# Kernel optimization log

Measured on AMD Instinct MI355X. Metric: run time of the kernel, lower is better.

Reference implementation:

```python
import jax, jax.numpy as jnp
import numpy as np

B_, C, N, M, DX = 4, 8, 1024, 1024, 1
POINTS_PER_UNIT = 64


def setup_inputs() -> dict:
    key = jax.random.key(0)
    k1, k2, k3 = jax.random.split(key, 3)
    xz = jax.random.uniform(k1, (M, DX), dtype=jnp.float32)          # grid locations
    z = jax.random.normal(k2, (B_, C, M, M), dtype=jnp.float32)      # grid encoding
    x = jax.random.normal(k3, (B_, N, DX), dtype=jnp.float32)        # target locations
    log_scale = jnp.log(jnp.float32(2.0 / POINTS_PER_UNIT))          # learned scalar
    return {"xz": xz, "z": z, "x": x, "log_scale": log_scale}


def reference(xz, z, x, log_scale):
    # pairwise squared distances: (b, n, m)
    dists2 = jnp.sum((x[:, :, None, :] - xz[None, None, :, :]) ** 2, axis=-1)
    # RBF weights
    weights = jnp.exp(-0.5 * dists2 / jnp.exp(2.0 * log_scale))      # (b, n, m)
    # weighted interpolation of grid encoding: (b, c, n, m)
    z1 = jnp.einsum("bnm,bcmk->bcnk", weights, z)
    # outer product z1 @ z1^T: (b, c, n, n)
    z2 = jnp.einsum("bcnk,bcok->bcno", z1, z1)
    return (xz, z2)
```

## Files before the change

kernel.cpp:

```cpp
#include <hip/hip_runtime.h>
#include <hip/hip_bf16.h>


typedef __attribute__((ext_vector_type(8))) unsigned short u16x8;
typedef __attribute__((ext_vector_type(8))) __bf16 bf16x8;
typedef __attribute__((ext_vector_type(4))) float f32x4;

typedef __attribute__((address_space(1))) void gvoid;
typedef __attribute__((address_space(3))) void svoid;
#define GLDS(g, s) __builtin_amdgcn_global_load_lds((gvoid*)(g), (svoid*)(s), 16, 0, 0)
#define BAR() asm volatile("s_barrier" ::: "memory")

__device__ __forceinline__ unsigned short f2bf(float f) {
  unsigned int u = __builtin_bit_cast(unsigned int, f);
  u += 0x7fffu + ((u >> 16) & 1u);
  return (unsigned short)(u >> 16);
}

__device__ __forceinline__ bf16x8 as_bf16x8(u16x8 v) {
  return __builtin_bit_cast(bf16x8, v);
}

__global__ void weights_kernel(const float* __restrict__ xz, const float* __restrict__ x,
                               const float* __restrict__ ls, unsigned short* __restrict__ W) {
  int bn = blockIdx.x;
  float xv = x[bn];
  float coef = -0.5f * __expf(-2.0f * ls[0]);
  unsigned short* Wrow = W + (size_t)bn * 1024;
  #pragma unroll
  for (int i = 0; i < 4; ++i) {
    int m = threadIdx.x + i * 256;
    float d = xv - xz[m];
    Wrow[m] = f2bf(__expf(coef * d * d));
  }
}

__global__ void transpose_kernel(const float* __restrict__ Z, unsigned short* __restrict__ Zt) {
  __shared__ float tile[64][65];
  int bc = blockIdx.z;
  const float* Zp = Z + ((size_t)bc << 20);
  unsigned short* Ztp = Zt + ((size_t)bc << 20);
  int m0 = blockIdx.x * 64, k0 = blockIdx.y * 64;
  int tx = threadIdx.x & 63, tg = threadIdx.x >> 6;
  #pragma unroll
  for (int i = 0; i < 16; ++i) {
    int ml = tg + i * 4;
    tile[ml][tx] = Zp[(size_t)(m0 + ml) * 1024 + k0 + tx];
  }
  __syncthreads();
  int tx2 = (threadIdx.x & 31) * 2, kg = threadIdx.x >> 5;
  #pragma unroll
  for (int i = 0; i < 8; ++i) {
    int kl = kg + i * 8;
    ushort2 v;
    v.x = f2bf(tile[tx2][kl]);
    v.y = f2bf(tile[tx2 + 1][kl]);
    *(ushort2*)&Ztp[(size_t)(k0 + kl) * 1024 + m0 + tx2] = v;
  }
}

template<bool OUT_BF16, bool A_PER_B>
__global__ __launch_bounds__(512, 2)
void gemm_nt8(const unsigned short* __restrict__ A, const unsigned short* __restrict__ B,
              unsigned short* __restrict__ Cbf, float* __restrict__ Cf) {
  extern __shared__ __align__(16) char smem[];

  const int bid = blockIdx.x;
  const int w = ((bid & 7) << 6) + (bid >> 3);
  const int bc = w >> 4;
  const int t  = w & 15;
  const int bi = t & 3, bj = t >> 2;

  const unsigned short* Ap = A + ((size_t)(A_PER_B ? (bc >> 3) : bc) << 20);
  const unsigned short* Bp = B + ((size_t)bc << 20);
  const int tid = threadIdx.x;
  const int wv = tid >> 6, lane = tid & 63;
  const int wr = wv >> 2, wc = wv & 3;
  const int la = lane & 15, ha = lane >> 4;

  f32x4 acc[8][4] = {};

  const unsigned short* gA0 = Ap + (size_t)(bi*256 +       wv*16 + (lane>>2)) * 1024 + (lane&3)*8;
  const unsigned short* gA1 = Ap + (size_t)(bi*256 + 128 + wv*16 + (lane>>2)) * 1024 + (lane&3)*8;
  const unsigned short* gB0 = Bp + (size_t)(bj*256 +       wv*16 + (lane>>2)) * 1024 + (lane&3)*8;
  const unsigned short* gB1 = Bp + (size_t)(bj*256 + 128 + wv*16 + (lane>>2)) * 1024 + (lane&3)*8;
  const int ldsw = wv * 1024;

  auto stageA = [&](int d, int kh, int kt) {
    const int ko = kt * 64 + kh * 32;
    char* dst = smem + d * 32768 + kh * 16384 + ldsw;
    GLDS(gA0 + ko, dst); GLDS(gA1 + ko, dst + 8192);
  };
  auto stageB = [&](int d, int kh, int kt) {
    const int ko = kt * 64 + kh * 32;
    char* dst = smem + 65536 + d * 32768 + kh * 16384 + ldsw;
    GLDS(gB0 + ko, dst); GLDS(gB1 + ko, dst + 8192);
  };

  const int abase = (wr * 128 + la) * 64 + ha * 16;
  const int bbase = 65536 + (wc * 64 + la) * 64 + ha * 16;

  u16x8 af[4], bfr[4];
  auto lda = [&](int d, int kh, int ms) {
    const char* p = smem + d * 32768 + kh * 16384 + ms * 4096 + abase;
    af[0] = *(const u16x8*)(p);
    af[1] = *(const u16x8*)(p + 1024);
    af[2] = *(const u16x8*)(p + 2048);
    af[3] = *(const u16x8*)(p + 3072);
  };
  auto ldb = [&](int d, int kh) {
    const char* p = smem + d * 32768 + kh * 16384 + bbase;
    bfr[0] = *(const u16x8*)(p);
    bfr[1] = *(const u16x8*)(p + 1024);
    bfr[2] = *(const u16x8*)(p + 2048);
    bfr[3] = *(const u16x8*)(p + 3072);
  };
  auto mfma16 = [&](int ms) {
    __builtin_amdgcn_s_setprio(1);
    #pragma unroll
    for (int i = 0; i < 4; ++i)
      #pragma unroll
      for (int n = 0; n < 4; ++n)
        acc[ms * 4 + i][n] = __builtin_amdgcn_mfma_f32_16x16x32_bf16(
            as_bf16x8(af[i]), as_bf16x8(bfr[n]), acc[ms * 4 + i][n], 0, 0, 0);
    __builtin_amdgcn_s_setprio(0);
  };

  stageA(0, 0, 0); stageB(0, 0, 0);
  stageA(0, 1, 0); stageB(0, 1, 0);
  stageA(1, 0, 1); stageB(1, 0, 1);
  asm volatile("s_waitcnt vmcnt(8)" ::: "memory");
  BAR();

  for (int tt = 0; tt < 16; ++tt) {
    const int d = tt & 1;
    if (tt < 15) stageA(d ^ 1, 1, tt + 1);
    ldb(d, 0); lda(d, 0, 0);
    BAR();
    mfma16(0);
    BAR();
    if (tt < 15) stageB(d ^ 1, 1, tt + 1);
    lda(d, 0, 1);
    BAR();
    mfma16(1);
    if (tt < 15) { asm volatile("s_waitcnt vmcnt(8)" ::: "memory"); }
    else         { asm volatile("s_waitcnt vmcnt(0)" ::: "memory"); }
    BAR();
    if (tt < 14) stageA(d, 0, tt + 2);
    ldb(d, 1); lda(d, 1, 0);
    BAR();
    mfma16(0);
    BAR();
    if (tt < 14) stageB(d, 0, tt + 2);
    lda(d, 1, 1);
    BAR();
    mfma16(1);
    if (tt < 14)       { asm volatile("s_waitcnt vmcnt(8)" ::: "memory"); }
    else if (tt == 14) { asm volatile("s_waitcnt vmcnt(4)" ::: "memory"); }
    BAR();
  }

  const size_t cb20 = (size_t)bc << 20;

  if (OUT_BF16) {
    unsigned short* sE = (unsigned short*)(smem) + wv * 1152;
    const int r2 = lane >> 2, ch = lane & 3;
    #pragma unroll
    for (int mb = 0; mb < 8; ++mb) {
      #pragma unroll
      for (int nb = 0; nb < 4; ++nb)
        #pragma unroll
        for (int j = 0; j < 4; ++j)
          sE[(ha * 4 + j) * 72 + nb * 16 + la] = f2bf(acc[mb][nb][j]);
      u16x8 v0 = *(const u16x8*)&sE[r2 * 72 + ch * 16];
      u16x8 v1 = *(const u16x8*)&sE[r2 * 72 + ch * 16 + 8];
      unsigned short* gp = Cbf + cb20 +
          (size_t)(bi * 256 + wr * 128 + mb * 16 + r2) * 1024 + bj * 256 + wc * 64 + ch * 16;
      *(u16x8*)gp = v0;
      *(u16x8*)(gp + 8) = v1;
    }
  } else {
    #pragma unroll
    for (int mb = 0; mb < 8; ++mb) {
      #pragma unroll
      for (int nb = 0; nb < 4; ++nb) {
        const int col = bj * 256 + wc * 64 + nb * 16 + la;
        #pragma unroll
        for (int j = 0; j < 4; ++j) {
          const int row = bi * 256 + wr * 128 + mb * 16 + ha * 4 + j;
          Cf[cb20 + (size_t)row * 1024 + col] = acc[mb][nb][j];
        }
      }
    }
  }
}

extern "C" void kernel_launch(void* const* d_in, const int* in_sizes, int n_in,
                              void* d_out, int out_size, void* d_ws, size_t ws_size,
                              hipStream_t stream) {
  const float* xz = (const float*)d_in[0];
  const float* z  = (const float*)d_in[1];
  const float* x  = (const float*)d_in[2];
  const float* ls = (const float*)d_in[3];
  float* out = (float*)d_out;

  unsigned short* W  = (unsigned short*)d_ws;
  unsigned short* Zt = W + ((size_t)4 << 20);
  unsigned short* z1 = Zt + ((size_t)32 << 20);

  hipFuncSetAttribute((const void*)gemm_nt8<true,  true >,
                      hipFuncAttributeMaxDynamicSharedMemorySize, 131072);
  hipFuncSetAttribute((const void*)gemm_nt8<false, false>,
                      hipFuncAttributeMaxDynamicSharedMemorySize, 131072);

  hipMemcpyAsync(out, xz, 1024 * sizeof(float), hipMemcpyDeviceToDevice, stream);
  weights_kernel<<<4096, 256, 0, stream>>>(xz, x, ls, W);
  transpose_kernel<<<dim3(16, 16, 32), 256, 0, stream>>>(z, Zt);
  gemm_nt8<true,  true ><<<512, 512, 131072, stream>>>(W,  Zt, z1, nullptr);
  gemm_nt8<false, false><<<512, 512, 131072, stream>>>(z1, z1, nullptr, out + 1024);
}
```

Measured before the change: 195.2 us.

## Exploit symmetry of z1·z1ᵀ with a dedicated upper-triangle GEMM and mirrored stores

Replaces the second full GEMM with a kernel that computes only the upper-triangular 256x128 tiles of each symmetric output and writes each off-diagonal tile twice, once transposed through LDS. This cuts the MFMA work of the second GEMM roughly in half. The fp32 epilogue now goes through LDS for vectorized, coalesced stores instead of scattered scalar writes. The cost is a smaller, differently shaped tile (256 threads, 48KB LDS, a full vmcnt(0) wait each k-step) and extra transpose stores for mirrored tiles.

```diff
diff --git a/kernel.cpp b/kernel.cpp
--- a/kernel.cpp
+++ b/kernel.cpp
@@ -59,10 +59,10 @@
   }
 }
 
-template<bool OUT_BF16, bool A_PER_B>
+template<bool A_PER_B>
 __global__ __launch_bounds__(512, 2)
 void gemm_nt8(const unsigned short* __restrict__ A, const unsigned short* __restrict__ B,
-              unsigned short* __restrict__ Cbf, float* __restrict__ Cf) {
+              unsigned short* __restrict__ Cbf) {
   extern __shared__ __align__(16) char smem[];
 
   const int bid = blockIdx.x;
@@ -136,61 +136,152 @@
     const int d = tt & 1;
     if (tt < 15) stageA(d ^ 1, 1, tt + 1);
     ldb(d, 0); lda(d, 0, 0);
-    BAR();
-    mfma16(0);
-    BAR();
+    BAR(); mfma16(0); BAR();
     if (tt < 15) stageB(d ^ 1, 1, tt + 1);
     lda(d, 0, 1);
-    BAR();
-    mfma16(1);
+    BAR(); mfma16(1);
     if (tt < 15) { asm volatile("s_waitcnt vmcnt(8)" ::: "memory"); }
     else         { asm volatile("s_waitcnt vmcnt(0)" ::: "memory"); }
     BAR();
     if (tt < 14) stageA(d, 0, tt + 2);
     ldb(d, 1); lda(d, 1, 0);
-    BAR();
-    mfma16(0);
-    BAR();
+    BAR(); mfma16(0); BAR();
     if (tt < 14) stageB(d, 0, tt + 2);
     lda(d, 1, 1);
-    BAR();
-    mfma16(1);
+    BAR(); mfma16(1);
     if (tt < 14)       { asm volatile("s_waitcnt vmcnt(8)" ::: "memory"); }
     else if (tt == 14) { asm volatile("s_waitcnt vmcnt(4)" ::: "memory"); }
     BAR();
   }
 
   const size_t cb20 = (size_t)bc << 20;
-
-  if (OUT_BF16) {
-    unsigned short* sE = (unsigned short*)(smem) + wv * 1152;
-    const int r2 = lane >> 2, ch = lane & 3;
-    #pragma unroll
-    for (int mb = 0; mb < 8; ++mb) {
+  unsigned short* sE = (unsigned short*)(smem) + wv * 1152;
+  const int r2 = lane >> 2, ch = lane & 3;
+  #pragma unroll
+  for (int mb = 0; mb < 8; ++mb) {
+    #pragma unroll
+    for (int nb = 0; nb < 4; ++nb)
+      #pragma unroll
+      for (int j = 0; j < 4; ++j)
+        sE[(ha * 4 + j) * 72 + nb * 16 + la] = f2bf(acc[mb][nb][j]);
+    u16x8 v0 = *(const u16x8*)&sE[r2 * 72 + ch * 16];
+    u16x8 v1 = *(const u16x8*)&sE[r2 * 72 + ch * 16 + 8];
+    unsigned short* gp = Cbf + cb20 +
+        (size_t)(bi * 256 + wr * 128 + mb * 16 + r2) * 1024 + bj * 256 + wc * 64 + ch * 16;
+    *(u16x8*)gp = v0;
+    *(u16x8*)(gp + 8) = v1;
+  }
+}
+
+__global__ __launch_bounds__(256, 2)
+void gemm2_sym(const unsigned short* __restrict__ Z1, float* __restrict__ Cf) {
+  __shared__ __align__(16) char smem[49152];
+
+  const int chunk = 80;
+  int w = ((int)blockIdx.x & 7) * chunk + ((int)blockIdx.x >> 3);
+  const int bc = w / 20;
+  int t = w % 20;
+  int bi = 0, cnt = 8;
+  while (t >= cnt) { t -= cnt; ++bi; cnt -= 2; }
+  const int bj = t + 2 * bi;
+  const bool pure = (bj >= 2 * bi + 2);
+
+  const unsigned short* Ap = Z1 + ((size_t)bc << 20);
+  const int tid = threadIdx.x;
+  const int wv = tid >> 6, lane = tid & 63;
+  const int wr = wv >> 1, wc = wv & 1;
+  const int la = lane & 15, ha = lane >> 4;
+
+  f32x4 acc[8][4] = {};
+
+  const int srow = wv * 16 + (lane >> 2);
+  const int scol = (lane & 3) * 8;
+  const unsigned short* gA = Ap + (size_t)(bi * 256 + srow) * 1024 + scol;
+  const unsigned short* gB = Ap + (size_t)(bj * 128 + srow) * 1024 + scol;
+  char* dA = smem + wv * 1024;
+  char* dB = smem + 32768 + wv * 1024;
+
+  auto stage = [&](int d, int tt2) {
+    const int ko = tt2 * 32;
+    GLDS(gA + ko,               dA + d * 16384);
+    GLDS(gA + ko +  64 * 1024,  dA + d * 16384 + 4096);
+    GLDS(gA + ko + 128 * 1024,  dA + d * 16384 + 8192);
+    GLDS(gA + ko + 192 * 1024,  dA + d * 16384 + 12288);
+    GLDS(gB + ko,               dB + d * 8192);
+    GLDS(gB + ko +  64 * 1024,  dB + d * 8192 + 4096);
+  };
+
+  const int abase = wr * 8192 + la * 64 + ha * 16;
+  const int bbase = 32768 + (wc * 64 + la) * 64 + ha * 16;
+  u16x8 af[4], bfr[4];
+  auto lda = [&](int d, int ms) {
+    const char* p = smem + d * 16384 + ms * 4096 + abase;
+    af[0] = *(const u16x8*)(p);
+    af[1] = *(const u16x8*)(p + 1024);
+    af[2] = *(const u16x8*)(p + 2048);
+    af[3] = *(const u16x8*)(p + 3072);
+  };
+  auto ldb = [&](int d) {
+    const char* p = smem + d * 8192 + bbase;
+    bfr[0] = *(const u16x8*)(p);
+    bfr[1] = *(const u16x8*)(p + 1024);
+    bfr[2] = *(const u16x8*)(p + 2048);
+    bfr[3] = *(const u16x8*)(p + 3072);
+  };
+  auto mfma16 = [&](int ms) {
+    __builtin_amdgcn_s_setprio(1);
+    #pragma unroll
+    for (int i = 0; i < 4; ++i)
+      #pragma unroll
+      for (int n = 0; n < 4; ++n)
+        acc[ms * 4 + i][n] = __builtin_amdgcn_mfma_f32_16x16x32_bf16(
+            as_bf16x8(af[i]), as_bf16x8(bfr[n]), acc[ms * 4 + i][n], 0, 0, 0);
+    __builtin_amdgcn_s_setprio(0);
+  };
+
+  stage(0, 0);
+  asm volatile("s_waitcnt vmcnt(0)" ::: "memory");
+  BAR();
+  for (int tt2 = 0; tt2 < 32; ++tt2) {
+    const int d = tt2 & 1;
+    if (tt2 < 31) stage(d ^ 1, tt2 + 1);
+    ldb(d); lda(d, 0);
+    BAR(); mfma16(0); BAR();
+    lda(d, 1);
+    BAR(); mfma16(1);
+    if (tt2 < 31) asm volatile("s_waitcnt vmcnt(0)" ::: "memory");
+    BAR();
+  }
+
+  const size_t cb20 = (size_t)bc << 20;
+  float* sF = (float*)(smem + wv * 12288);
+  float* sM = (float*)(smem + wv * 12288 + 6144);
+  const int rr = lane >> 2, cch = (lane & 3) * 16;
+
+  #pragma unroll
+  for (int mb = 0; mb < 8; ++mb) {
+    #pragma unroll
+    for (int nb = 0; nb < 4; ++nb)
+      #pragma unroll
+      for (int j = 0; j < 4; ++j)
+        sF[(ha * 4 + j) * 68 + nb * 16 + la] = acc[mb][nb][j];
+    float* gp = Cf + cb20 +
+        (size_t)(bi * 256 + wr * 128 + mb * 16 + rr) * 1024 + bj * 128 + wc * 64 + cch;
+    #pragma unroll
+    for (int q = 0; q < 4; ++q)
+      *(f32x4*)(gp + q * 4) = *(const f32x4*)&sF[rr * 68 + cch + q * 4];
+
+    if (pure) {
       #pragma unroll
       for (int nb = 0; nb < 4; ++nb)
         #pragma unroll
         for (int j = 0; j < 4; ++j)
-          sE[(ha * 4 + j) * 72 + nb * 16 + la] = f2bf(acc[mb][nb][j]);
-      u16x8 v0 = *(const u16x8*)&sE[r2 * 72 + ch * 16];
-      u16x8 v1 = *(const u16x8*)&sE[r2 * 72 + ch * 16 + 8];
-      unsigned short* gp = Cbf + cb20 +
-          (size_t)(bi * 256 + wr * 128 + mb * 16 + r2) * 1024 + bj * 256 + wc * 64 + ch * 16;
-      *(u16x8*)gp = v0;
-      *(u16x8*)(gp + 8) = v1;
-    }
-  } else {
-    #pragma unroll
-    for (int mb = 0; mb < 8; ++mb) {
-      #pragma unroll
-      for (int nb = 0; nb < 4; ++nb) {
-        const int col = bj * 256 + wc * 64 + nb * 16 + la;
-        #pragma unroll
-        for (int j = 0; j < 4; ++j) {
-          const int row = bi * 256 + wr * 128 + mb * 16 + ha * 4 + j;
-          Cf[cb20 + (size_t)row * 1024 + col] = acc[mb][nb][j];
-        }
-      }
+          sM[(nb * 16 + la) * 20 + ha * 4 + j] = acc[mb][nb][j];
+      float* mp = Cf + cb20 +
+          (size_t)(bj * 128 + wc * 64 + lane) * 1024 + bi * 256 + wr * 128 + mb * 16;
+      #pragma unroll
+      for (int q = 0; q < 4; ++q)
+        *(f32x4*)(mp + q * 4) = *(const f32x4*)&sM[lane * 20 + q * 4];
     }
   }
 }
@@ -208,14 +299,12 @@
   unsigned short* Zt = W + ((size_t)4 << 20);
   unsigned short* z1 = Zt + ((size_t)32 << 20);
 
-  hipFuncSetAttribute((const void*)gemm_nt8<true,  true >,
-                      hipFuncAttributeMaxDynamicSharedMemorySize, 131072);
-  hipFuncSetAttribute((const void*)gemm_nt8<false, false>,
+  hipFuncSetAttribute((const void*)gemm_nt8<true>,
                       hipFuncAttributeMaxDynamicSharedMemorySize, 131072);
 
   hipMemcpyAsync(out, xz, 1024 * sizeof(float), hipMemcpyDeviceToDevice, stream);
   weights_kernel<<<4096, 256, 0, stream>>>(xz, x, ls, W);
   transpose_kernel<<<dim3(16, 16, 32), 256, 0, stream>>>(z, Zt);
-  gemm_nt8<true,  true ><<<512, 512, 131072, stream>>>(W,  Zt, z1, nullptr);
-  gemm_nt8<false, false><<<512, 512, 131072, stream>>>(z1, z1, nullptr, out + 1024);
-}
+  gemm_nt8<true><<<512, 512, 131072, stream>>>(W, Zt, z1);
+  gemm2_sym<<<640, 256, 0, stream>>>(z1, out + 1024);
+}
```

Result: slower. 204.7 us (+4.9%).

## Exploit symmetry of z1·z1ᵀ with a triangular-tile second GEMM kernel

Applied to the files above, without the earlier changes.

Replaces the second full GEMM with a dedicated kernel that computes only the upper-triangular 128x128 tiles of each symmetric z1·z1ᵀ output and writes each off-diagonal tile twice, once directly and once transposed through shared memory. This roughly halves the MFMA work and operand loads of the second GEMM. The new kernel also uses smaller tiles, a swizzled LDS layout and a three-slot load pipeline. In exchange it adds an LDS transpose and extra barriers in the epilogue, and smaller tiles reuse each loaded operand less.

```diff
diff --git a/kernel.cpp b/kernel.cpp
--- a/kernel.cpp
+++ b/kernel.cpp
@@ -59,10 +59,10 @@
   }
 }
 
-template<bool OUT_BF16, bool A_PER_B>
+template<bool A_PER_B>
 __global__ __launch_bounds__(512, 2)
 void gemm_nt8(const unsigned short* __restrict__ A, const unsigned short* __restrict__ B,
-              unsigned short* __restrict__ Cbf, float* __restrict__ Cf) {
+              unsigned short* __restrict__ Cbf) {
   extern __shared__ __align__(16) char smem[];
 
   const int bid = blockIdx.x;
@@ -136,61 +136,152 @@
     const int d = tt & 1;
     if (tt < 15) stageA(d ^ 1, 1, tt + 1);
     ldb(d, 0); lda(d, 0, 0);
-    BAR();
-    mfma16(0);
-    BAR();
+    BAR(); mfma16(0); BAR();
     if (tt < 15) stageB(d ^ 1, 1, tt + 1);
     lda(d, 0, 1);
-    BAR();
-    mfma16(1);
+    BAR(); mfma16(1);
     if (tt < 15) { asm volatile("s_waitcnt vmcnt(8)" ::: "memory"); }
     else         { asm volatile("s_waitcnt vmcnt(0)" ::: "memory"); }
     BAR();
     if (tt < 14) stageA(d, 0, tt + 2);
     ldb(d, 1); lda(d, 1, 0);
-    BAR();
-    mfma16(0);
-    BAR();
+    BAR(); mfma16(0); BAR();
     if (tt < 14) stageB(d, 0, tt + 2);
     lda(d, 1, 1);
-    BAR();
-    mfma16(1);
+    BAR(); mfma16(1);
     if (tt < 14)       { asm volatile("s_waitcnt vmcnt(8)" ::: "memory"); }
     else if (tt == 14) { asm volatile("s_waitcnt vmcnt(4)" ::: "memory"); }
     BAR();
   }
 
   const size_t cb20 = (size_t)bc << 20;
-
-  if (OUT_BF16) {
-    unsigned short* sE = (unsigned short*)(smem) + wv * 1152;
-    const int r2 = lane >> 2, ch = lane & 3;
-    #pragma unroll
-    for (int mb = 0; mb < 8; ++mb) {
-      #pragma unroll
-      for (int nb = 0; nb < 4; ++nb)
+  unsigned short* sE = (unsigned short*)(smem) + wv * 1152;
+  const int r2 = lane >> 2, ch = lane & 3;
+  #pragma unroll
+  for (int mb = 0; mb < 8; ++mb) {
+    #pragma unroll
+    for (int nb = 0; nb < 4; ++nb)
+      #pragma unroll
+      for (int j = 0; j < 4; ++j)
+        sE[(ha * 4 + j) * 72 + nb * 16 + la] = f2bf(acc[mb][nb][j]);
+    u16x8 v0 = *(const u16x8*)&sE[r2 * 72 + ch * 16];
+    u16x8 v1 = *(const u16x8*)&sE[r2 * 72 + ch * 16 + 8];
+    unsigned short* gp = Cbf + cb20 +
+        (size_t)(bi * 256 + wr * 128 + mb * 16 + r2) * 1024 + bj * 256 + wc * 64 + ch * 16;
+    *(u16x8*)gp = v0;
+    *(u16x8*)(gp + 8) = v1;
+  }
+}
+
+__global__ __launch_bounds__(256, 3)
+void gemm2_sym(const unsigned short* __restrict__ A, float* __restrict__ Cf) {
+  __shared__ __align__(16) char smem[49152];
+
+  const int chunk = 144;
+  int w = ((int)blockIdx.x & 7) * chunk + ((int)blockIdx.x >> 3);
+  int bc = w / 36;
+  int t  = w % 36;
+  int bi = 0;
+  while (t >= 8 - bi) { t -= 8 - bi; ++bi; }
+  int bj = bi + t;
+
+  const unsigned short* Ap = A + ((size_t)bc << 20);
+  const int tid = threadIdx.x;
+  const int wave = tid >> 6, lane = tid & 63;
+  const int wr = wave >> 1, wc = wave & 1;
+  const int la = lane & 15, ha = lane >> 4;
+  f32x4 acc[4][4] = {};
+
+  const int slog = (lane & 7) ^ ((lane >> 3) & 7);
+  const int rloc = 2 * (lane >> 3) + (slog & 1);
+  const int cloc = (slog >> 1) * 8;
+  const unsigned short* gA0 = Ap + (size_t)(bi * 128 + (wave * 2)     * 16 + rloc) * 1024 + cloc;
+  const unsigned short* gA1 = Ap + (size_t)(bi * 128 + (wave * 2 + 1) * 16 + rloc) * 1024 + cloc;
+  const unsigned short* gB0 = Ap + (size_t)(bj * 128 + (wave * 2)     * 16 + rloc) * 1024 + cloc;
+  const unsigned short* gB1 = Ap + (size_t)(bj * 128 + (wave * 2 + 1) * 16 + rloc) * 1024 + cloc;
+
+  auto stage = [&](int slot, int kt) {
+    char* dA = smem + slot * 8192 + wave * 2048;
+    char* dB = smem + 24576 + slot * 8192 + wave * 2048;
+    GLDS(gA0 + kt, dA); GLDS(gA1 + kt, dA + 1024);
+    GLDS(gB0 + kt, dB); GLDS(gB1 + kt, dB + 1024);
+  };
+
+  const int sphys = ((ha << 1) | (la & 1)) ^ (la >> 1);
+  const int aoff = wr * 4096 + (la >> 1) * 128 + sphys * 16;
+  const int boff = wc * 4096 + (la >> 1) * 128 + sphys * 16;
+
+  auto compute = [&](int slot) {
+    const char* rA = smem + slot * 8192;
+    const char* rB = smem + 24576 + slot * 8192;
+    u16x8 af[4], bfr[4];
+    #pragma unroll
+    for (int m = 0; m < 4; ++m) af[m]  = *(const u16x8*)(rA + aoff + m * 1024);
+    #pragma unroll
+    for (int n = 0; n < 4; ++n) bfr[n] = *(const u16x8*)(rB + boff + n * 1024);
+    #pragma unroll
+    for (int m = 0; m < 4; ++m)
+      #pragma unroll
+      for (int n = 0; n < 4; ++n)
+        acc[m][n] = __builtin_amdgcn_mfma_f32_16x16x32_bf16(
+            as_bf16x8(af[m]), as_bf16x8(bfr[n]), acc[m][n], 0, 0, 0);
+  };
+
+  stage(0, 0);
+  stage(1, 32);
+  asm volatile("s_waitcnt vmcnt(4)" ::: "memory");
+  __builtin_amdgcn_s_barrier();
+  int sl0 = 0, sl1 = 1, sl2 = 2;
+  for (int t2 = 0; t2 < 32; ++t2) {
+    if (t2 < 30) stage(sl2, (t2 + 2) * 32);
+    compute(sl0);
+    if (t2 < 30)       asm volatile("s_waitcnt vmcnt(4)" ::: "memory");
+    else if (t2 == 30) asm volatile("s_waitcnt vmcnt(0)" ::: "memory");
+    if (t2 < 31) __builtin_amdgcn_s_barrier();
+    int tmp = sl0; sl0 = sl1; sl1 = sl2; sl2 = tmp;
+  }
+  __builtin_amdgcn_s_barrier();
+
+  const size_t cb20 = (size_t)bc << 20;
+
+  #pragma unroll
+  for (int m = 0; m < 4; ++m) {
+    int row0 = bi * 128 + wr * 64 + m * 16 + ha * 4;
+    #pragma unroll
+    for (int n = 0; n < 4; ++n) {
+      int col = bj * 128 + wc * 64 + n * 16 + la;
+      #pragma unroll
+      for (int j = 0; j < 4; ++j)
+        Cf[cb20 + (size_t)(row0 + j) * 1024 + col] = acc[m][n][j];
+    }
+  }
+  if (bi != bj) {
+    float (*sT)[129] = (float(*)[129])smem;
+    #pragma unroll
+    for (int b = 0; b < 4; ++b) {
+      if (wr == (b >> 1)) {
         #pragma unroll
-        for (int j = 0; j < 4; ++j)
-          sE[(ha * 4 + j) * 72 + nb * 16 + la] = f2bf(acc[mb][nb][j]);
-      u16x8 v0 = *(const u16x8*)&sE[r2 * 72 + ch * 16];
-      u16x8 v1 = *(const u16x8*)&sE[r2 * 72 + ch * 16 + 8];
-      unsigned short* gp = Cbf + cb20 +
-          (size_t)(bi * 256 + wr * 128 + mb * 16 + r2) * 1024 + bj * 256 + wc * 64 + ch * 16;
-      *(u16x8*)gp = v0;
-      *(u16x8*)(gp + 8) = v1;
-    }
-  } else {
-    #pragma unroll
-    for (int mb = 0; mb < 8; ++mb) {
-      #pragma unroll
-      for (int nb = 0; nb < 4; ++nb) {
-        const int col = bj * 256 + wc * 64 + nb * 16 + la;
-        #pragma unroll
-        for (int j = 0; j < 4; ++j) {
-          const int row = bi * 256 + wr * 128 + mb * 16 + ha * 4 + j;
-          Cf[cb20 + (size_t)row * 1024 + col] = acc[mb][nb][j];
+        for (int dm = 0; dm < 2; ++dm) {
+          int m = (b & 1) * 2 + dm;
+          #pragma unroll
+          for (int n = 0; n < 4; ++n)
+            #pragma unroll
+            for (int j = 0; j < 4; ++j)
+              sT[dm * 16 + ha * 4 + j][wc * 64 + n * 16 + la] = acc[m][n][j];
         }
       }
+      __syncthreads();
+      int c  = tid >> 1;
+      int r0 = (tid & 1) * 16;
+      float* gp = Cf + cb20 + (size_t)(bj * 128 + c) * 1024 + bi * 128 + b * 32 + r0;
+      #pragma unroll
+      for (int q = 0; q < 4; ++q) {
+        f32x4 v;
+        #pragma unroll
+        for (int k = 0; k < 4; ++k) v[k] = sT[r0 + q * 4 + k][c];
+        *(f32x4*)(gp + q * 4) = v;
+      }
+      __syncthreads();
     }
   }
 }
@@ -208,14 +299,12 @@
   unsigned short* Zt = W + ((size_t)4 << 20);
   unsigned short* z1 = Zt + ((size_t)32 << 20);
 
-  hipFuncSetAttribute((const void*)gemm_nt8<true,  true >,
-                      hipFuncAttributeMaxDynamicSharedMemorySize, 131072);
-  hipFuncSetAttribute((const void*)gemm_nt8<false, false>,
+  hipFuncSetAttribute((const void*)gemm_nt8<true>,
                       hipFuncAttributeMaxDynamicSharedMemorySize, 131072);
 
   hipMemcpyAsync(out, xz, 1024 * sizeof(float), hipMemcpyDeviceToDevice, stream);
   weights_kernel<<<4096, 256, 0, stream>>>(xz, x, ls, W);
   transpose_kernel<<<dim3(16, 16, 32), 256, 0, stream>>>(z, Zt);
-  gemm_nt8<true,  true ><<<512, 512, 131072, stream>>>(W,  Zt, z1, nullptr);
-  gemm_nt8<false, false><<<512, 512, 131072, stream>>>(z1, z1, nullptr, out + 1024);
-}
+  gemm_nt8<true><<<512, 512, 131072, stream>>>(W, Zt, z1);
+  gemm2_sym<<<32 * 36, 256, 0, stream>>>(z1, out + 1024);
+}
```

Measured after the change: 182.2 us. 6.6% less time.
